# Optimization experiments

Measured on AMD Instinct MI355X. Metric: run time of the kernel, lower is better.

## Reference

```python
import jax, jax.numpy as jnp
import numpy as np

P1 = np.array([[700.0, 0.0, 128.0, 102400.0], [0.0, 700.0, 128.0, 102400.0], [0.0, 0.0, 1.0, 800.0]])
P2 = np.array([[-128.0, 0.0, 700.0, 102400.0], [-128.0, 700.0, 0.0, 102400.0], [-1.0, 0.0, 0.0, 800.0]])


def _calculate_fundamental_matrix(P_src, P_dst):
    # camera center of source view = right null vector of P_src
    _, _, Vt = np.linalg.svd(P_src)
    C = Vt[-1]
    C = C / C[-1]
    e2 = P_dst @ C  # epipole in destination view
    ex = np.array([[0.0, -e2[2], e2[1]], [e2[2], 0.0, -e2[0]], [-e2[1], e2[0], 0.0]])
    F = ex @ P_dst @ np.linalg.pinv(P_src)
    return F / np.linalg.norm(F)  # scale-invariant for epipolar lines


def setup_inputs() -> dict:
    key = jax.random.key(0)
    x = jax.random.normal(key, (2, 8, 256, 256), dtype=jnp.float32)
    F21 = jnp.asarray(_calculate_fundamental_matrix(P1, P2), dtype=jnp.float32)
    return {"input": x, "F": F21}


def _translate(img, F):
    # For each output pixel p=(u,v,1) (destination view), the epipolar line in the
    # source image is l = F^T p (since x_dst^T F x_src = 0). The kernel integrates
    # (nearest-neighbor line rasterization, dominant-axis sweep) the source image
    # along that line -> output (B,C,H,W).
    B, C, Hs, Ws = img.shape
    Ho, Wo = Hs, Ws
    uu, vv = jnp.meshgrid(jnp.arange(Wo, dtype=img.dtype), jnp.arange(Ho, dtype=img.dtype))  # (Ho,Wo)
    p = jnp.stack([uu, vv, jnp.ones_like(uu)])            # (3,Ho,Wo) homogeneous pixels
    l = jnp.einsum('ji,jhw->ihw', F, p)                    # F^T p -> line coeffs (3,Ho,Wo)
    a, b, c = l[0], l[1], l[2]
    eps = jnp.asarray(1e-8, img.dtype)
    b_safe = jnp.where(jnp.abs(b) < eps, eps, b)
    a_safe = jnp.where(jnp.abs(a) < eps, eps, a)
    zeros = jnp.zeros((B, C, Ho, Wo), img.dtype)

    def col_step(acc, x):
        xf = x.astype(img.dtype)
        y = -(a * xf + c) / b_safe                         # (Ho,Wo)
        yi = jnp.round(y).astype(jnp.int32)
        valid = (yi >= 0) & (yi < Hs)
        samp = img[:, :, jnp.clip(yi, 0, Hs - 1), x]       # gather -> (B,C,Ho,Wo)
        return acc + jnp.where(valid, samp, jnp.zeros((), img.dtype)), None

    def row_step(acc, y):
        yf = y.astype(img.dtype)
        x = -(b * yf + c) / a_safe                         # (Ho,Wo)
        xi = jnp.round(x).astype(jnp.int32)
        valid = (xi >= 0) & (xi < Ws)
        samp = img[:, :, y, jnp.clip(xi, 0, Ws - 1)]       # gather -> (B,C,Ho,Wo)
        return acc + jnp.where(valid, samp, jnp.zeros((), img.dtype)), None

    sum_col, _ = jax.lax.scan(col_step, zeros, jnp.arange(Ws))
    sum_row, _ = jax.lax.scan(row_step, zeros, jnp.arange(Hs))
    use_col = jnp.abs(b) >= jnp.abs(a)                     # dominant-axis selection per pixel
    return jnp.where(use_col, sum_col, sum_row)


def reference(input, F):
    assert input.ndim == 4
    return _translate(input, F)
```

## Files before the change

### kernel.cpp

```cpp
#include <hip/hip_runtime.h>
#include <hip/hip_fp16.h>

#define HS 256
#define WSZ 256
#define NPIX (HS * WSZ)
#define NCH 16
#define NELEM (NPIX * NCH)

typedef float f4 __attribute__((ext_vector_type(4)));

__global__ __launch_bounds__(256) void transpose_f16(const float* __restrict__ x,
                                                     __half* __restrict__ T) {
    __shared__ float lds[16][257];
    int tid  = threadIdx.x;
    int base = blockIdx.x * 256;
#pragma unroll
    for (int ch = 0; ch < 16; ++ch)
        lds[ch][tid] = x[ch * NPIX + base + tid];
    if (blockIdx.x == 0 && tid < 128)
        ((unsigned int*)(T + NELEM))[tid] = 0u;
    __syncthreads();
    uint2* T2 = (uint2*)T;
#pragma unroll
    for (int it = 0; it < 4; ++it) {
        int idx = it * 256 + tid;
        int p   = idx >> 2;
        int q   = idx & 3;
        __half2 a = __floats2half2_rn(lds[q * 4 + 0][p], lds[q * 4 + 1][p]);
        __half2 b = __floats2half2_rn(lds[q * 4 + 2][p], lds[q * 4 + 3][p]);
        uint2 o;
        o.x = __builtin_bit_cast(unsigned int, a);
        o.y = __builtin_bit_cast(unsigned int, b);
        T2[base * 4 + idx] = o;
    }
}

struct LineGeom {
    float p, q, c;
    bool  col;
};

__device__ __forceinline__ LineGeom make_geom(const float* __restrict__ F, int pix) {
#pragma clang fp contract(off)
    int w = pix & (WSZ - 1);
    int h = pix >> 8;
    float u = (float)w, v = (float)h;
    float a = __builtin_fmaf(F[3], v, F[0] * u) + F[6];
    float b = __builtin_fmaf(F[4], v, F[1] * u) + F[7];
    float c = __builtin_fmaf(F[5], v, F[2] * u) + F[8];
    const float eps = 1e-8f;
    float bs = (fabsf(b) < eps) ? eps : b;
    float as = (fabsf(a) < eps) ? eps : a;
    LineGeom g;
    g.col = (fabsf(b) >= fabsf(a));
    g.p   = g.col ? a : b;
    g.q   = g.col ? bs : as;
    g.c   = c;
    return g;
}

__device__ __forceinline__ int chainY(const LineGeom& g, int s) {
#pragma clang fp contract(off)
    float t  = __builtin_fmaf(g.p, (float)s, g.c);
    float y  = (-t) / g.q;
    return (int)__builtin_rintf(y);
}

__device__ __forceinline__ f4 h4f4(uint2 v) {
    float2 a = __half22float2(__builtin_bit_cast(__half2, v.x));
    float2 b = __half22float2(__builtin_bit_cast(__half2, v.y));
    f4 r = {a.x, a.y, b.x, b.y};
    return r;
}

#define QUAD_BCAST(dst, src, ctrl)                                              \
    dst = __builtin_amdgcn_mov_dpp(src, ctrl, 0xf, 0xf, false)

__global__ __launch_bounds__(256) void epi_gather_f16(const uint2* __restrict__ T2,
                                                      const float* __restrict__ x,
                                                      const float* __restrict__ F,
                                                      float* __restrict__ out) {
    int tid  = blockIdx.x * 256 + threadIdx.x;
    int quad = tid & 3;
    int sq   = (tid >> 2) & 3;
    int pix  = tid >> 4;

    LineGeom g = make_geom(F, pix);
    f4 acc = {0.f, 0.f, 0.f, 0.f};

    if (g.col) {
        const int zeroU2 = NPIX * 4 + quad;
        int schain = (sq << 6) + quad;
        int sPart  = ((sq << 6) << 2) | quad;

#pragma unroll 2
        for (int m = 0; m < 8; ++m) {
            int t0 = chainY(g, schain); schain += 4;
            int t1 = chainY(g, schain); schain += 4;
            int fb[8];
            int tj;
#define IDX(J, SRC, CTRL)                                                       \
            QUAD_BCAST(tj, SRC, CTRL);                                          \
            fb[J] = (tj << 10) | sPart;                                         \
            fb[J] = ((unsigned)tj < 256u) ? fb[J] : (zeroU2 - 4 * (J));
            IDX(0, t0, 0x00) IDX(1, t0, 0x55) IDX(2, t0, 0xAA) IDX(3, t0, 0xFF)
            IDX(4, t1, 0x00) IDX(5, t1, 0x55) IDX(6, t1, 0xAA) IDX(7, t1, 0xFF)
#undef IDX
            uint2 v0 = T2[fb[0] +  0], v1 = T2[fb[1] +  4];
            uint2 v2 = T2[fb[2] +  8], v3 = T2[fb[3] + 12];
            uint2 v4 = T2[fb[4] + 16], v5 = T2[fb[5] + 20];
            uint2 v6 = T2[fb[6] + 24], v7 = T2[fb[7] + 28];
            acc += h4f4(v0); acc += h4f4(v1); acc += h4f4(v2); acc += h4f4(v3);
            acc += h4f4(v4); acc += h4f4(v5); acc += h4f4(v6); acc += h4f4(v7);
            sPart += 32;
        }
    } else {
        int lo = sq << 6;
        int ch = quad * 4;
        for (int s = lo; s < lo + 64; ++s) {
            int xi = chainY(g, s);
            if ((unsigned)xi < 256u) {
                int addr = s * WSZ + xi;
                acc.x += x[(ch + 0) * NPIX + addr];
                acc.y += x[(ch + 1) * NPIX + addr];
                acc.z += x[(ch + 2) * NPIX + addr];
                acc.w += x[(ch + 3) * NPIX + addr];
            }
        }
    }

    acc.x += __shfl_xor(acc.x, 8, 64);
    acc.y += __shfl_xor(acc.y, 8, 64);
    acc.z += __shfl_xor(acc.z, 8, 64);
    acc.w += __shfl_xor(acc.w, 8, 64);
    acc.x += __shfl_xor(acc.x, 4, 64);
    acc.y += __shfl_xor(acc.y, 4, 64);
    acc.z += __shfl_xor(acc.z, 4, 64);
    acc.w += __shfl_xor(acc.w, 4, 64);

    if (sq == 0) {
        int ch = quad * 4;
        out[(ch + 0) * NPIX + pix] = acc.x;
        out[(ch + 1) * NPIX + pix] = acc.y;
        out[(ch + 2) * NPIX + pix] = acc.z;
        out[(ch + 3) * NPIX + pix] = acc.w;
    }
}

__global__ __launch_bounds__(256) void epi_gather_direct(const float* __restrict__ x,
                                                         const float* __restrict__ F,
                                                         float* __restrict__ out) {
    int tid  = blockIdx.x * 256 + threadIdx.x;
    int quad = tid & 3;
    int pix  = tid >> 2;

    LineGeom g = make_geom(F, pix);

    float4 acc = make_float4(0.f, 0.f, 0.f, 0.f);
    int base = quad * 4;

#pragma unroll 2
    for (int s = 0; s < 256; ++s) {
        int  yi    = chainY(g, s);
        bool valid = ((unsigned)yi < 256u);
        int  tcl   = valid ? yi : 0;
        int  addr  = g.col ? (tcl * WSZ + s) : (s * WSZ + tcl);
        if (valid) {
            acc.x += x[(base + 0) * NPIX + addr];
            acc.y += x[(base + 1) * NPIX + addr];
            acc.z += x[(base + 2) * NPIX + addr];
            acc.w += x[(base + 3) * NPIX + addr];
        }
    }

    out[(base + 0) * NPIX + pix] = acc.x;
    out[(base + 1) * NPIX + pix] = acc.y;
    out[(base + 2) * NPIX + pix] = acc.z;
    out[(base + 3) * NPIX + pix] = acc.w;
}

extern "C" void kernel_launch(void* const* d_in, const int* in_sizes, int n_in,
                              void* d_out, int out_size, void* d_ws, size_t ws_size,
                              hipStream_t stream) {
    const float* x   = (const float*)d_in[0];
    const float* F   = (const float*)d_in[1];
    float*       out = (float*)d_out;

    const size_t need = (size_t)NELEM * sizeof(__half) + 512;
    if (ws_size >= need) {
        __half* T = (__half*)d_ws;
        transpose_f16<<<NPIX / 256, 256, 0, stream>>>(x, T);
        epi_gather_f16<<<(NPIX * 16) / 256, 256, 0, stream>>>((const uint2*)T, x, F, out);
    } else {
        epi_gather_direct<<<(NPIX * 4) / 256, 256, 0, stream>>>(x, F, out);
    }
}
```

Before: 91.87 us.

## Gather 16-byte fp16 vectors per lane with 8-way step split and precomputed rows

Each pixel's 16 lanes are now split as 8 step-phases times 2 channel halves. Each lane loads a uint4 (8 half channels) per step instead of a uint2, and the DPP quad broadcast of line coordinates is dropped. All 32 line coordinates are precomputed into registers up front, and the cross-lane reduction grows to three shuffle stages over 8 accumulators. The aim is fewer, wider gather loads and no DPP traffic. The cost is more registers, which may lower occupancy, and more shuffles.

Result: no change. 92.60 us (+0.8%).

```diff
diff --git a/kernel.cpp b/kernel.cpp
--- a/kernel.cpp
+++ b/kernel.cpp
@@ -66,84 +66,104 @@
     return (int)__builtin_rintf(y);
 }
 
-__device__ __forceinline__ f4 h4f4(uint2 v) {
-    float2 a = __half22float2(__builtin_bit_cast(__half2, v.x));
-    float2 b = __half22float2(__builtin_bit_cast(__half2, v.y));
-    f4 r = {a.x, a.y, b.x, b.y};
-    return r;
-}
-
-#define QUAD_BCAST(dst, src, ctrl)                                              \
-    dst = __builtin_amdgcn_mov_dpp(src, ctrl, 0xf, 0xf, false)
-
-__global__ __launch_bounds__(256) void epi_gather_f16(const uint2* __restrict__ T2,
+__device__ __forceinline__ void acc16(uint4 v, f4& a0, f4& a1) {
+    float2 p0 = __half22float2(__builtin_bit_cast(__half2, v.x));
+    float2 p1 = __half22float2(__builtin_bit_cast(__half2, v.y));
+    float2 p2 = __half22float2(__builtin_bit_cast(__half2, v.z));
+    float2 p3 = __half22float2(__builtin_bit_cast(__half2, v.w));
+    f4 u0 = {p0.x, p0.y, p1.x, p1.y};
+    f4 u1 = {p2.x, p2.y, p3.x, p3.y};
+    a0 += u0;
+    a1 += u1;
+}
+
+__global__ __launch_bounds__(256) void epi_gather_f16(const uint4* __restrict__ Tq,
                                                       const float* __restrict__ x,
                                                       const float* __restrict__ F,
                                                       float* __restrict__ out) {
-    int tid  = blockIdx.x * 256 + threadIdx.x;
-    int quad = tid & 3;
-    int sq   = (tid >> 2) & 3;
-    int pix  = tid >> 4;
+    int tid = blockIdx.x * 256 + threadIdx.x;
+    int r   = tid & 15;
+    int k   = r >> 1;
+    int h   = r & 1;
+    int pix = tid >> 4;
 
     LineGeom g = make_geom(F, pix);
-    f4 acc = {0.f, 0.f, 0.f, 0.f};
+    f4 a0 = {0.f, 0.f, 0.f, 0.f};
+    f4 a1 = {0.f, 0.f, 0.f, 0.f};
 
     if (g.col) {
-        const int zeroU2 = NPIX * 4 + quad;
-        int schain = (sq << 6) + quad;
-        int sPart  = ((sq << 6) << 2) | quad;
-
-#pragma unroll 2
-        for (int m = 0; m < 8; ++m) {
-            int t0 = chainY(g, schain); schain += 4;
-            int t1 = chainY(g, schain); schain += 4;
-            int fb[8];
-            int tj;
-#define IDX(J, SRC, CTRL)                                                       \
-            QUAD_BCAST(tj, SRC, CTRL);                                          \
-            fb[J] = (tj << 10) | sPart;                                         \
-            fb[J] = ((unsigned)tj < 256u) ? fb[J] : (zeroU2 - 4 * (J));
-            IDX(0, t0, 0x00) IDX(1, t0, 0x55) IDX(2, t0, 0xAA) IDX(3, t0, 0xFF)
-            IDX(4, t1, 0x00) IDX(5, t1, 0x55) IDX(6, t1, 0xAA) IDX(7, t1, 0xFF)
-#undef IDX
-            uint2 v0 = T2[fb[0] +  0], v1 = T2[fb[1] +  4];
-            uint2 v2 = T2[fb[2] +  8], v3 = T2[fb[3] + 12];
-            uint2 v4 = T2[fb[4] + 16], v5 = T2[fb[5] + 20];
-            uint2 v6 = T2[fb[6] + 24], v7 = T2[fb[7] + 28];
-            acc += h4f4(v0); acc += h4f4(v1); acc += h4f4(v2); acc += h4f4(v3);
-            acc += h4f4(v4); acc += h4f4(v5); acc += h4f4(v6); acc += h4f4(v7);
-            sPart += 32;
+        int ych[32];
+#pragma unroll
+        for (int m = 0; m < 32; ++m) ych[m] = chainY(g, 8 * m + k);
+
+        const int PADB = NPIX * 2;
+        int padr = PADB + r;
+        int rb   = r;
+
+#pragma unroll
+        for (int b = 0; b < 4; ++b) {
+            int adr[8];
+#pragma unroll
+            for (int j = 0; j < 8; ++j) {
+                int y  = ych[8 * b + j];
+                int av = (int)((unsigned)y << 9) + rb;
+                adr[j] = ((unsigned)y < 256u) ? av : (padr - 16 * j);
+            }
+            uint4 v0 = Tq[adr[0] +   0];
+            uint4 v1 = Tq[adr[1] +  16];
+            uint4 v2 = Tq[adr[2] +  32];
+            uint4 v3 = Tq[adr[3] +  48];
+            uint4 v4 = Tq[adr[4] +  64];
+            uint4 v5 = Tq[adr[5] +  80];
+            uint4 v6 = Tq[adr[6] +  96];
+            uint4 v7 = Tq[adr[7] + 112];
+            acc16(v0, a0, a1); acc16(v1, a0, a1);
+            acc16(v2, a0, a1); acc16(v3, a0, a1);
+            acc16(v4, a0, a1); acc16(v5, a0, a1);
+            acc16(v6, a0, a1); acc16(v7, a0, a1);
+            rb += 128;
         }
     } else {
-        int lo = sq << 6;
-        int ch = quad * 4;
-        for (int s = lo; s < lo + 64; ++s) {
+        int ch0 = h * 8;
+        for (int m = 0; m < 32; ++m) {
+            int s  = 8 * m + k;
             int xi = chainY(g, s);
             if ((unsigned)xi < 256u) {
                 int addr = s * WSZ + xi;
-                acc.x += x[(ch + 0) * NPIX + addr];
-                acc.y += x[(ch + 1) * NPIX + addr];
-                acc.z += x[(ch + 2) * NPIX + addr];
-                acc.w += x[(ch + 3) * NPIX + addr];
+                a0.x += x[(ch0 + 0) * NPIX + addr];
+                a0.y += x[(ch0 + 1) * NPIX + addr];
+                a0.z += x[(ch0 + 2) * NPIX + addr];
+                a0.w += x[(ch0 + 3) * NPIX + addr];
+                a1.x += x[(ch0 + 4) * NPIX + addr];
+                a1.y += x[(ch0 + 5) * NPIX + addr];
+                a1.z += x[(ch0 + 6) * NPIX + addr];
+                a1.w += x[(ch0 + 7) * NPIX + addr];
             }
         }
     }
 
-    acc.x += __shfl_xor(acc.x, 8, 64);
-    acc.y += __shfl_xor(acc.y, 8, 64);
-    acc.z += __shfl_xor(acc.z, 8, 64);
-    acc.w += __shfl_xor(acc.w, 8, 64);
-    acc.x += __shfl_xor(acc.x, 4, 64);
-    acc.y += __shfl_xor(acc.y, 4, 64);
-    acc.z += __shfl_xor(acc.z, 4, 64);
-    acc.w += __shfl_xor(acc.w, 4, 64);
-
-    if (sq == 0) {
-        int ch = quad * 4;
-        out[(ch + 0) * NPIX + pix] = acc.x;
-        out[(ch + 1) * NPIX + pix] = acc.y;
-        out[(ch + 2) * NPIX + pix] = acc.z;
-        out[(ch + 3) * NPIX + pix] = acc.w;
+#pragma unroll
+    for (int d = 2; d <= 8; d <<= 1) {
+        a0.x += __shfl_xor(a0.x, d, 64);
+        a0.y += __shfl_xor(a0.y, d, 64);
+        a0.z += __shfl_xor(a0.z, d, 64);
+        a0.w += __shfl_xor(a0.w, d, 64);
+        a1.x += __shfl_xor(a1.x, d, 64);
+        a1.y += __shfl_xor(a1.y, d, 64);
+        a1.z += __shfl_xor(a1.z, d, 64);
+        a1.w += __shfl_xor(a1.w, d, 64);
+    }
+
+    if ((r & 14) == 0) {
+        int ch0 = h * 8;
+        out[(ch0 + 0) * NPIX + pix] = a0.x;
+        out[(ch0 + 1) * NPIX + pix] = a0.y;
+        out[(ch0 + 2) * NPIX + pix] = a0.z;
+        out[(ch0 + 3) * NPIX + pix] = a0.w;
+        out[(ch0 + 4) * NPIX + pix] = a1.x;
+        out[(ch0 + 5) * NPIX + pix] = a1.y;
+        out[(ch0 + 6) * NPIX + pix] = a1.z;
+        out[(ch0 + 7) * NPIX + pix] = a1.w;
     }
 }
 
@@ -190,7 +210,7 @@
     if (ws_size >= need) {
         __half* T = (__half*)d_ws;
         transpose_f16<<<NPIX / 256, 256, 0, stream>>>(x, T);
-        epi_gather_f16<<<(NPIX * 16) / 256, 256, 0, stream>>>((const uint2*)T, x, F, out);
+        epi_gather_f16<<<(NPIX * 16) / 256, 256, 0, stream>>>((const uint4*)T, x, F, out);
     } else {
         epi_gather_direct<<<(NPIX * 4) / 256, 256, 0, stream>>>(x, F, out);
     }
```
